# Kernel optimization log

Measured on AMD Instinct MI355X. Metric: run time of the kernel, lower is better.

## Reference

```python
import jax, jax.numpy as jnp
import numpy as np

P = 30000    # pathway graph nodes
E = 480000   # edges
G = 20000    # genes
MP = 32      # max pathways per gene (padded)
R = 28       # pathway root count
B = 4096     # batch of gene pairs
IN, H, OUT = 394, 256, 64
GD = 128     # params.gene_dim


def setup_inputs() -> dict:
    key = jax.random.key(0)
    ks = iter(jax.random.split(key, 48))
    nx = lambda shape, s=1.0: jax.random.normal(next(ks), shape, dtype=jnp.float32) * s
    inp = {}
    inp["x1"] = nx((P, IN))
    inp["x2"] = nx((P, IN))
    inp["edge_src"] = jax.random.randint(next(ks), (E,), 0, P)
    inp["edge_dst"] = jax.random.randint(next(ks), (E,), 0, P)
    inp["edge_weight"] = jax.random.uniform(next(ks), (E,), dtype=jnp.float32)
    for g in ("g1", "g2"):
        inp[g + "_w1"] = nx((IN, H), 0.05); inp[g + "_b1"] = jnp.zeros((H,), jnp.float32)
        inp[g + "_w2"] = nx((H, OUT), 0.05); inp[g + "_b2"] = jnp.zeros((OUT,), jnp.float32)
    inp["pl1_w"] = nx((OUT * R, 256), 0.02); inp["pl1_b"] = jnp.zeros((256,), jnp.float32)
    inp["bn1_g"] = jnp.ones((256,), jnp.float32); inp["bn1_b"] = jnp.zeros((256,), jnp.float32)
    inp["pl2_w"] = nx((256, GD), 0.05); inp["pl2_b"] = jnp.zeros((GD,), jnp.float32)
    inp["bn2_g"] = jnp.ones((GD,), jnp.float32); inp["bn2_b"] = jnp.zeros((GD,), jnp.float32)
    inp["fc_w"] = nx((2 * GD, 256), 0.05); inp["fc_b"] = jnp.zeros((256,), jnp.float32)
    inp["fc1_w"] = nx((256, 128), 0.05); inp["fc1_b"] = jnp.zeros((128,), jnp.float32)
    inp["fc2_w"] = nx((128, 1), 0.05); inp["fc2_b"] = jnp.zeros((1,), jnp.float32)
    inp["pathway_root"] = jax.random.randint(next(ks), (P,), 0, R)
    inp["gene_paths"] = jax.random.randint(next(ks), (G, MP), 0, P)
    inp["gene_paths_mask"] = jax.random.uniform(next(ks), (G, MP)) < 0.7
    inp["head_ids"] = jax.random.randint(next(ks), (B,), 0, G)
    inp["tail_ids"] = jax.random.randint(next(ks), (B,), 0, G)
    return inp


def gcn_conv(x, w, b, src, dst, ew):
    # PyG GCNConv with edge weights + self loops (fill_value=1), symmetric norm.
    h = x @ w
    deg = jnp.zeros((x.shape[0],), x.dtype).at[dst].add(ew) + 1.0
    norm = jax.lax.rsqrt(deg)
    msg = h[src] * (ew * norm[src] * norm[dst])[:, None]
    agg = jnp.zeros_like(h).at[dst].add(msg) + h * (norm * norm)[:, None]
    return agg + b


def pathway_gcn(x, w1, b1, w2, b2, src, dst, ew):
    h = jax.nn.relu(gcn_conv(x, w1, b1, src, dst, ew))  # F.dropout in eval = identity
    return gcn_conv(h, w2, b2, src, dst, ew)


def gene_pathway_feat(s, gene_ids, gene_paths, gene_paths_mask, pathway_root):
    # Vectorized form of the per-gene python-loop gather + per-root sum.
    paths = gene_paths[gene_ids]                      # [B, MP]
    m = gene_paths_mask[gene_ids].astype(s.dtype)     # [B, MP]
    gathered = s[paths]                               # [B, MP, 64]
    oh = jax.nn.one_hot(pathway_root[paths], R, dtype=s.dtype) * m[..., None]
    feat = jnp.einsum('bpr,bpd->brd', oh, gathered)   # segment-sum into roots
    return feat.reshape(paths.shape[0], R * s.shape[1])


def batchnorm(x, g, b, eps=1e-5):
    mu = x.mean(0)
    var = x.var(0)  # biased, as torch BN training
    return g * (x - mu) * jax.lax.rsqrt(var + eps) + b


def reference(x1, x2, edge_src, edge_dst, edge_weight,
              g1_w1, g1_b1, g1_w2, g1_b2, g2_w1, g2_b1, g2_w2, g2_b2,
              pl1_w, pl1_b, bn1_g, bn1_b, pl2_w, pl2_b, bn2_g, bn2_b,
              fc_w, fc_b, fc1_w, fc1_b, fc2_w, fc2_b,
              pathway_root, gene_paths, gene_paths_mask, head_ids, tail_ids):
    out1 = pathway_gcn(x1, g1_w1, g1_b1, g1_w2, g1_b2, edge_src, edge_dst, edge_weight)
    out2 = pathway_gcn(x2, g2_w1, g2_b1, g2_w2, g2_b2, edge_src, edge_dst, edge_weight)
    s = out1 + out2  # original stacks feats from both graphs per pathway, then sums

    def fuse(ids):
        f = gene_pathway_feat(s, ids, gene_paths, gene_paths_mask, pathway_root)
        h = jax.nn.relu(batchnorm(f @ pl1_w + pl1_b, bn1_g, bn1_b))
        return batchnorm(h @ pl2_w + pl2_b, bn2_g, bn2_b)

    fuse_feat = jnp.concatenate([fuse(head_ids), fuse(tail_ids)], axis=1)  # [B, 2*GD]
    final = jax.nn.relu(fuse_feat @ fc_w + fc_b) @ fc1_w + fc1_b
    return jax.nn.relu(final) @ fc2_w + fc2_b  # [B, 1]
```

## Files before the change

kernel.cpp:

```cpp
#include <hip/hip_runtime.h>
#include <cstdint>

typedef __attribute__((ext_vector_type(4))) float f32x4;
typedef __attribute__((ext_vector_type(8))) short s16x8;

__device__ inline unsigned short f2bf(float f) {
    unsigned u = __float_as_uint(f);
    unsigned r = (u + 0x7FFFu + ((u >> 16) & 1u)) >> 16;
    return (unsigned short)r;
}
__device__ inline float b2f(unsigned short h) {
    return __uint_as_float(((unsigned)h) << 16);
}

__device__ inline void gload16(const unsigned short* g, unsigned short* l) {
    __builtin_amdgcn_global_load_lds(
        (const __attribute__((address_space(1))) unsigned int*)g,
        (__attribute__((address_space(3))) unsigned int*)l, 16, 0, 0);
}

struct TD { const float* in; unsigned short* out; int K, N, Kp, ldo; };

__global__ void prep_kernel(const unsigned char* __restrict__ mask, int maskBytes,
                            int* __restrict__ flag, float* __restrict__ zspan, long long zwords,
                            TD d0, TD d1, TD d2, TD d3, TD d4, TD d5, TD d6, TD d7) {
    int y = blockIdx.y;
    if (y == 0) {
        if (blockIdx.x != 0) return;
        __shared__ int isByte, isFloat;
        if (threadIdx.x == 0) { isByte = 0; isFloat = 0; }
        __syncthreads();
        const unsigned* w = (const unsigned*)mask;
        for (int i = threadIdx.x; i < maskBytes / 4; i += blockDim.x) {
            unsigned v = w[i];
            if (v == 0u || v == 1u) continue;
            if (v == 0x3f800000u) isFloat = 1; else isByte = 1;
        }
        __syncthreads();
        if (threadIdx.x == 0) *flag = isFloat ? 2 : (isByte ? 1 : 0);
        return;
    }
    if (y == 1) {
        long long i = (long long)blockIdx.x * 256 + threadIdx.x;
        if (i < zwords) zspan[i] = 0.f;
        return;
    }
    TD d = d0;
    if (y == 3) d = d1; else if (y == 4) d = d2; else if (y == 5) d = d3;
    else if (y == 6) d = d4; else if (y == 7) d = d5; else if (y == 8) d = d6; else if (y == 9) d = d7;
    int idx = blockIdx.x * 256 + threadIdx.x;
    if (idx >= d.N * d.Kp) return;
    int n = idx / d.Kp, k = idx - n * d.Kp;
    d.out[(size_t)n * d.ldo + k] = (k < d.K) ? f2bf(d.in[(size_t)k * d.N + n]) : (unsigned short)0;
}

__global__ void deg_cnt_kernel(const int* __restrict__ dst, const float* __restrict__ ew,
                               float* __restrict__ degw, int* __restrict__ cnt, int E) {
    int e = blockIdx.x * 256 + threadIdx.x;
    if (e >= E) return;
    int d = dst[e];
    unsafeAtomicAdd(&degw[d], ew[e]);
    atomicAdd(&cnt[d], 1);
}

__global__ __launch_bounds__(1024) void norm_scan_kernel(const int* __restrict__ cnt,
                                                         int* __restrict__ rowstart,
                                                         float* __restrict__ degw, int P) {
    int t = threadIdx.x;
    if (blockIdx.x > 0) {
        int i = (blockIdx.x - 1) * 1024 + t;
        if (i < P) degw[i] = rsqrtf(degw[i] + 1.0f);
        return;
    }
    __shared__ int wsum[16];
    __shared__ int carry;
    int lane = t & 63, w = t >> 6;
    if (t == 0) { carry = 0; rowstart[0] = 0; }
    __syncthreads();
    for (int base = 0; base < P; base += 1024) {
        int v = (base + t < P) ? cnt[base + t] : 0;
        int x = v;
#pragma unroll
        for (int off = 1; off < 64; off <<= 1) {
            int y2 = __shfl_up(x, off);
            if (lane >= off) x += y2;
        }
        if (lane == 63) wsum[w] = x;
        __syncthreads();
        if (w == 0) {
            int xs = (lane < 16) ? wsum[lane] : 0;
#pragma unroll
            for (int off = 1; off < 16; off <<= 1) {
                int y2 = __shfl_up(xs, off);
                if (lane >= off) xs += y2;
            }
            if (lane < 16) wsum[lane] = xs;
        }
        __syncthreads();
        int wbase = (w == 0) ? 0 : wsum[w - 1];
        int inc = carry + wbase + x;
        if (base + t < P) rowstart[base + t + 1] = inc;
        __syncthreads();
        if (t == 1023) carry = inc;
        __syncthreads();
    }
}

__global__ void fill_kernel(const int* __restrict__ src, const int* __restrict__ dst,
                            const float* __restrict__ ew, const float* __restrict__ norm,
                            const int* __restrict__ rowstart, int* __restrict__ fill,
                            int* __restrict__ csrc, float* __restrict__ coef, int E) {
    int e = blockIdx.x * 256 + threadIdx.x;
    if (e >= E) return;
    int d = dst[e], sI = src[e];
    int pos = rowstart[d] + atomicAdd(&fill[d], 1);
    csrc[pos] = sI;
    coef[pos] = ew[e] * norm[sI] * norm[d];
}

__global__ __launch_bounds__(256) void conv1_agg_kernel(
    const unsigned short* __restrict__ Hb, const float* __restrict__ norm,
    const int* __restrict__ rowstart, const int* __restrict__ csrc, const float* __restrict__ coef,
    const float* __restrict__ b0, const float* __restrict__ b1,
    unsigned short* __restrict__ out, int P) {
    int node = blockIdx.x * 4 + (threadIdx.x >> 6);
    if (node >= P) return;
    int z = blockIdx.y;
    const unsigned short* H = Hb + (size_t)z * P * 256;
    const float* bias = z ? b1 : b0;
    int lane = threadIdx.x & 63;
    int f4 = lane * 4;
    float nn = norm[node];
    ushort4 hv = *(const ushort4*)(H + (size_t)node * 256 + f4);
    float a0 = b2f(hv.x) * nn * nn, a1 = b2f(hv.y) * nn * nn;
    float a2 = b2f(hv.z) * nn * nn, a3 = b2f(hv.w) * nn * nn;
    int s0 = rowstart[node], s1 = rowstart[node + 1];
    int p = s0;
    for (; p + 4 <= s1; p += 4) {
        int i0 = csrc[p], i1 = csrc[p + 1], i2 = csrc[p + 2], i3 = csrc[p + 3];
        float c0 = coef[p], c1 = coef[p + 1], c2 = coef[p + 2], c3 = coef[p + 3];
        ushort4 v0 = *(const ushort4*)(H + (size_t)i0 * 256 + f4);
        ushort4 v1 = *(const ushort4*)(H + (size_t)i1 * 256 + f4);
        ushort4 v2 = *(const ushort4*)(H + (size_t)i2 * 256 + f4);
        ushort4 v3 = *(const ushort4*)(H + (size_t)i3 * 256 + f4);
        a0 += b2f(v0.x) * c0 + b2f(v1.x) * c1 + b2f(v2.x) * c2 + b2f(v3.x) * c3;
        a1 += b2f(v0.y) * c0 + b2f(v1.y) * c1 + b2f(v2.y) * c2 + b2f(v3.y) * c3;
        a2 += b2f(v0.z) * c0 + b2f(v1.z) * c1 + b2f(v2.z) * c2 + b2f(v3.z) * c3;
        a3 += b2f(v0.w) * c0 + b2f(v1.w) * c1 + b2f(v2.w) * c2 + b2f(v3.w) * c3;
    }
    for (; p < s1; ++p) {
        int i0 = csrc[p];
        float c0 = coef[p];
        ushort4 v0 = *(const ushort4*)(H + (size_t)i0 * 256 + f4);
        a0 += b2f(v0.x) * c0; a1 += b2f(v0.y) * c0; a2 += b2f(v0.z) * c0; a3 += b2f(v0.w) * c0;
    }
    float4 bv = *(const float4*)(bias + f4);
    ushort4 o;
    o.x = f2bf(fmaxf(a0 + bv.x, 0.f));
    o.y = f2bf(fmaxf(a1 + bv.y, 0.f));
    o.z = f2bf(fmaxf(a2 + bv.z, 0.f));
    o.w = f2bf(fmaxf(a3 + bv.w, 0.f));
    *(ushort4*)(out + (size_t)node * 512 + z * 256 + f4) = o;
}

__global__ __launch_bounds__(256) void conv2_agg_kernel(
    const unsigned short* __restrict__ T, const float* __restrict__ norm,
    const int* __restrict__ rowstart, const int* __restrict__ csrc, const float* __restrict__ coef,
    const float* __restrict__ b0, const float* __restrict__ b1,
    float* __restrict__ s, int P) {
    int node = blockIdx.x * 4 + (threadIdx.x >> 6);
    if (node >= P) return;
    int lane = threadIdx.x & 63;
    float nn = norm[node];
    float acc = b2f(T[(size_t)node * 64 + lane]) * nn * nn;
    int s0 = rowstart[node], s1 = rowstart[node + 1];
    int p = s0;
    for (; p + 4 <= s1; p += 4) {
        int i0 = csrc[p], i1 = csrc[p + 1], i2 = csrc[p + 2], i3 = csrc[p + 3];
        float c0 = coef[p], c1 = coef[p + 1], c2 = coef[p + 2], c3 = coef[p + 3];
        acc += b2f(T[(size_t)i0 * 64 + lane]) * c0 + b2f(T[(size_t)i1 * 64 + lane]) * c1 +
               b2f(T[(size_t)i2 * 64 + lane]) * c2 + b2f(T[(size_t)i3 * 64 + lane]) * c3;
    }
    for (; p < s1; ++p) acc += b2f(T[(size_t)csrc[p] * 64 + lane]) * coef[p];
    s[(size_t)node * 64 + lane] = acc + b0[lane] + b1[lane];
}

struct G2 {
    const void* A[2]; const unsigned short* Bt[2]; const float* bias[2];
    float* Cf[2]; unsigned short* Cb[2];
};

template<int BM, int BN, int WM, int WN>
__global__ __launch_bounds__(256) void gemm1_hybrid_kernel(
    const float* __restrict__ x0, const float* __restrict__ x1,
    const unsigned short* __restrict__ Bt0, const unsigned short* __restrict__ Bt1,
    unsigned short* __restrict__ C0, unsigned short* __restrict__ C1,
    int M, int IN, int Kp, int ldc) {
    const int z = blockIdx.z;
    const float* A = z ? x1 : x0;
    const unsigned short* Bt = z ? Bt1 : Bt0;
    unsigned short* Cb = z ? C1 : C0;

    constexpr int LDK = 40;
    __shared__ __align__(16) unsigned short As[2][BM * LDK];
    __shared__ __align__(16) unsigned short Bs[2][BN * 32];
    const int t = threadIdx.x, lane = t & 63, wid = t >> 6;
    constexpr int NWC = BN / WN;
    const int wr = wid / NWC, wc = wid % NWC;
    constexpr int MR = WM / 16, NR = WN / 16;
    static_assert((BM / WM) * (BN / WN) == 4, "4 waves");
    constexpr int BI = BN / 64;
    const int row0 = blockIdx.y * BM, col0 = blockIdx.x * BN;
    const int sr = lane >> 2;
    const int sc = ((lane & 3) ^ ((lane >> 3) & 3)) * 8;
    int brow[BI];
#pragma unroll
    for (int i = 0; i < BI; ++i) brow[i] = col0 + (wid * BI + i) * 16 + sr;
    const int ar = t >> 2, akc = (t & 3) * 8;
    int arowg = row0 + ar; if (arowg >= M) arowg = M - 1;
    const float* aptr = A + (size_t)arowg * IN;

    f32x4 acc[MR][NR] = {};
    const int r16 = lane & 15, q = lane >> 4;
    const int kbA = q * 8;
    const int kbB = ((q ^ ((r16 >> 1) & 3)) * 8);

    auto stageB = [&](int buf, int kt) {
#pragma unroll
        for (int i = 0; i < BI; ++i)
            gload16(Bt + (size_t)brow[i] * Kp + kt + sc, &Bs[buf][(wid * BI + i) * 512]);
    };
    auto loadA = [&](int kt, float* v) {
        int kg = kt + akc;
        if (kg + 8 <= IN) {
            float2 a = *(const float2*)(aptr + kg);
            float2 b = *(const float2*)(aptr + kg + 2);
            float2 c = *(const float2*)(aptr + kg + 4);
            float2 d = *(const float2*)(aptr + kg + 6);
            v[0]=a.x; v[1]=a.y; v[2]=b.x; v[3]=b.y; v[4]=c.x; v[5]=c.y; v[6]=d.x; v[7]=d.y;
        } else {
#pragma unroll
            for (int j = 0; j < 8; ++j) v[j] = (kg + j < IN) ? aptr[kg + j] : 0.f;
        }
    };
    auto writeA = [&](int buf, const float* v) {
        s16x8 w;
#pragma unroll
        for (int j = 0; j < 8; ++j) w[j] = (short)f2bf(v[j]);
        *(s16x8*)&As[buf][ar * LDK + akc] = w;
    };

    {
        float v[8];
        stageB(0, 0);
        loadA(0, v);
        writeA(0, v);
    }
    int cur = 0;
    for (int kt = 0; kt < Kp; kt += 32) {
        __syncthreads();
        float nv[8];
        const bool has = (kt + 32 < Kp);
        if (has) { stageB(cur ^ 1, kt + 32); loadA(kt + 32, nv); }
        s16x8 af[MR], bfr[NR];
#pragma unroll
        for (int m = 0; m < MR; ++m)
            af[m] = *(const s16x8*)&As[cur][(wr * WM + m * 16 + r16) * LDK + kbA];
#pragma unroll
        for (int n = 0; n < NR; ++n)
            bfr[n] = *(const s16x8*)&Bs[cur][(wc * WN + n * 16 + r16) * 32 + kbB];
#pragma unroll
        for (int m = 0; m < MR; ++m)
#pragma unroll
            for (int n = 0; n < NR; ++n)
                acc[m][n] = __builtin_amdgcn_mfma_f32_16x16x32_bf16(af[m], bfr[n], acc[m][n], 0, 0, 0);
        if (has) writeA(cur ^ 1, nv);
        cur ^= 1;
    }
#pragma unroll
    for (int m = 0; m < MR; ++m)
#pragma unroll
        for (int n = 0; n < NR; ++n) {
            int col = col0 + wc * WN + n * 16 + r16;
#pragma unroll
            for (int r = 0; r < 4; ++r) {
                int row = row0 + wr * WM + m * 16 + q * 4 + r;
                if (row < M) Cb[(size_t)row * ldc + col] = f2bf(acc[m][n][r]);
            }
        }
}

template<int BM, int BN, int WM, int WN>
__global__ __launch_bounds__(256) void m97s_gemm_kernel(
    G2 g, int M, int Kp, int lda, int ldc, int relu) {
    const int z = blockIdx.z;
    const unsigned short* A = (const unsigned short*)(z ? g.A[1] : g.A[0]);
    const unsigned short* Bt = z ? g.Bt[1] : g.Bt[0];
    const float* bias = z ? g.bias[1] : g.bias[0];
    float* Cf = z ? g.Cf[1] : g.Cf[0];
    unsigned short* Cb = z ? g.Cb[1] : g.Cb[0];

    __shared__ __align__(16) unsigned short As[2][BM * 32];
    __shared__ __align__(16) unsigned short Bs[2][BN * 32];
    const int t = threadIdx.x, lane = t & 63, wid = t >> 6;
    constexpr int NWC = BN / WN;
    const int wr = wid / NWC, wc = wid % NWC;
    constexpr int MR = WM / 16, NR = WN / 16;
    static_assert((BM / WM) * (BN / WN) == 4, "4 waves");
    constexpr int AI = BM / 64, BI = BN / 64;
    const int row0 = blockIdx.y * BM, col0 = blockIdx.x * BN;
    const int sr = lane >> 2;
    const int sc = ((lane & 3) ^ ((lane >> 3) & 3)) * 8;
    int arow[AI];
#pragma unroll
    for (int i = 0; i < AI; ++i) {
        int r = row0 + (wid * AI + i) * 16 + sr;
        arow[i] = r < M ? r : M - 1;
    }
    int brow[BI];
#pragma unroll
    for (int i = 0; i < BI; ++i) brow[i] = col0 + (wid * BI + i) * 16 + sr;

    f32x4 acc[MR][NR] = {};
    const int r16 = lane & 15;
    const int kb = (((lane >> 4) ^ ((r16 >> 1) & 3)) * 8);

    auto stage = [&](int buf, int kt) {
#pragma unroll
        for (int i = 0; i < AI; ++i)
            gload16(A + (size_t)arow[i] * lda + kt + sc, &As[buf][(wid * AI + i) * 512]);
#pragma unroll
        for (int i = 0; i < BI; ++i)
            gload16(Bt + (size_t)brow[i] * Kp + kt + sc, &Bs[buf][(wid * BI + i) * 512]);
    };

    stage(0, 0);
    int cur = 0;
    for (int kt = 0; kt < Kp; kt += 32) {
        __syncthreads();
        if (kt + 32 < Kp) stage(cur ^ 1, kt + 32);
        s16x8 af[MR], bfr[NR];
#pragma unroll
        for (int m = 0; m < MR; ++m)
            af[m] = *(const s16x8*)&As[cur][(wr * WM + m * 16 + r16) * 32 + kb];
#pragma unroll
        for (int n = 0; n < NR; ++n)
            bfr[n] = *(const s16x8*)&Bs[cur][(wc * WN + n * 16 + r16) * 32 + kb];
#pragma unroll
        for (int m = 0; m < MR; ++m)
#pragma unroll
            for (int n = 0; n < NR; ++n)
                acc[m][n] = __builtin_amdgcn_mfma_f32_16x16x32_bf16(af[m], bfr[n], acc[m][n], 0, 0, 0);
        cur ^= 1;
    }
#pragma unroll
    for (int m = 0; m < MR; ++m)
#pragma unroll
        for (int n = 0; n < NR; ++n) {
            int col = col0 + wc * WN + n * 16 + r16;
#pragma unroll
            for (int r = 0; r < 4; ++r) {
                int row = row0 + wr * WM + m * 16 + (lane >> 4) * 4 + r;
                if (row < M) {
                    float v = acc[m][n][r] + (bias ? bias[col] : 0.f);
                    if (relu) v = fmaxf(v, 0.f);
                    if (Cf) Cf[(size_t)row * ldc + col] = v;
                    if (Cb) Cb[(size_t)row * ldc + col] = f2bf(v);
                }
            }
        }
}

template<int BM, int BN, int WM, int WN>
__global__ __launch_bounds__(256) void pl1_stats_kernel(
    G2 g, int M, int Kp, int lda, int ldc, float* __restrict__ statsPart, int C) {
    const int z = blockIdx.z;
    const unsigned short* A = (const unsigned short*)(z ? g.A[1] : g.A[0]);
    const unsigned short* Bt = z ? g.Bt[1] : g.Bt[0];
    const float* bias = z ? g.bias[1] : g.bias[0];
    float* Cf = z ? g.Cf[1] : g.Cf[0];

    __shared__ __align__(16) unsigned short As[2][BM * 32];
    __shared__ __align__(16) unsigned short Bs[2][BN * 32];
    const int t = threadIdx.x, lane = t & 63, wid = t >> 6;
    constexpr int NWC = BN / WN;
    const int wr = wid / NWC, wc = wid % NWC;
    constexpr int MR = WM / 16, NR = WN / 16;
    constexpr int AI = BM / 64, BI = BN / 64;
    const int row0 = blockIdx.y * BM, col0 = blockIdx.x * BN;
    const int sr = lane >> 2;
    const int sc = ((lane & 3) ^ ((lane >> 3) & 3)) * 8;
    int arow[AI];
#pragma unroll
    for (int i = 0; i < AI; ++i) {
        int r = row0 + (wid * AI + i) * 16 + sr;
        arow[i] = r < M ? r : M - 1;
    }
    int brow[BI];
#pragma unroll
    for (int i = 0; i < BI; ++i) brow[i] = col0 + (wid * BI + i) * 16 + sr;

    f32x4 acc[MR][NR] = {};
    const int r16 = lane & 15, q = lane >> 4;
    const int kb = ((q ^ ((r16 >> 1) & 3)) * 8);

    auto stage = [&](int buf, int kt) {
#pragma unroll
        for (int i = 0; i < AI; ++i)
            gload16(A + (size_t)arow[i] * lda + kt + sc, &As[buf][(wid * AI + i) * 512]);
#pragma unroll
        for (int i = 0; i < BI; ++i)
            gload16(Bt + (size_t)brow[i] * Kp + kt + sc, &Bs[buf][(wid * BI + i) * 512]);
    };

    stage(0, 0);
    int cur = 0;
    for (int kt = 0; kt < Kp; kt += 32) {
        __syncthreads();
        if (kt + 32 < Kp) stage(cur ^ 1, kt + 32);
        s16x8 af[MR], bfr[NR];
#pragma unroll
        for (int m = 0; m < MR; ++m)
            af[m] = *(const s16x8*)&As[cur][(wr * WM + m * 16 + r16) * 32 + kb];
#pragma unroll
        for (int n = 0; n < NR; ++n)
            bfr[n] = *(const s16x8*)&Bs[cur][(wc * WN + n * 16 + r16) * 32 + kb];
#pragma unroll
        for (int m = 0; m < MR; ++m)
#pragma unroll
            for (int n = 0; n < NR; ++n)
                acc[m][n] = __builtin_amdgcn_mfma_f32_16x16x32_bf16(af[m], bfr[n], acc[m][n], 0, 0, 0);
        cur ^= 1;
    }
    float* sp = statsPart + (size_t)z * 2 * C;
#pragma unroll
    for (int n = 0; n < NR; ++n) {
        int col = col0 + wc * WN + n * 16 + r16;
        float sm = 0.f, sq = 0.f;
#pragma unroll
        for (int m = 0; m < MR; ++m)
#pragma unroll
            for (int r = 0; r < 4; ++r) {
                int row = row0 + wr * WM + m * 16 + q * 4 + r;
                float v = acc[m][n][r] + bias[col];
                Cf[(size_t)row * ldc + col] = v;
                sm += v; sq += v * v;
            }
        sm += __shfl_xor(sm, 16); sq += __shfl_xor(sq, 16);
        sm += __shfl_xor(sm, 32); sq += __shfl_xor(sq, 32);
        if (lane < 16) {
            unsafeAtomicAdd(&sp[col], sm);
            unsafeAtomicAdd(&sp[C + col], sq);
        }
    }
}

template<int BM, int BN, int WM, int WN>
__global__ __launch_bounds__(256) void pl2_bn_stats_kernel(
    const float* __restrict__ z1, const unsigned short* __restrict__ Bt,
    const float* __restrict__ bias, float* __restrict__ z2,
    const float* __restrict__ bn1part, const float* __restrict__ bn1g, const float* __restrict__ bn1b,
    float* __restrict__ bn2part, int Mrows, int Kp, int ldc) {
    const int z = blockIdx.z;
    const float* A = z1 + (size_t)z * Mrows * Kp;
    float* Cf = z2 + (size_t)z * Mrows * ldc;

    constexpr int LDK = 40;
    __shared__ __align__(16) unsigned short As[BM * LDK];
    __shared__ __align__(16) unsigned short Bs[BN * 32];
    __shared__ float sc1[256], sh1[256];
    const int t = threadIdx.x, lane = t & 63, wid = t >> 6;
    {
        const float* bp = bn1part + (size_t)z * 2 * 256;
        float mu = bp[t] / Mrows;
        float var = bp[256 + t] / Mrows - mu * mu;
        float rstd = rsqrtf(var + 1e-5f);
        float s = rstd * bn1g[t];
        sc1[t] = s; sh1[t] = bn1b[t] - mu * s;
    }
    constexpr int NWC = BN / WN;
    const int wr = wid / NWC, wc = wid % NWC;
    constexpr int MR = WM / 16, NR = WN / 16;
    constexpr int BI = BN / 64;
    const int row0 = blockIdx.y * BM, col0 = blockIdx.x * BN;
    const int sr = lane >> 2;
    const int sc = ((lane & 3) ^ ((lane >> 3) & 3)) * 8;
    int brow[BI];
#pragma unroll
    for (int i = 0; i < BI; ++i) brow[i] = col0 + (wid * BI + i) * 16 + sr;
    const int ar = t >> 2, akc = (t & 3) * 8;
    const float* aptr = A + (size_t)(row0 + ar) * Kp;
    f32x4 acc[MR][NR] = {};
    const int r16 = lane & 15, q = lane >> 4;
    const int kbA = q * 8;
    const int kbB = ((q ^ ((r16 >> 1) & 3)) * 8);
    __syncthreads();

    for (int kt = 0; kt < Kp; kt += 32) {
#pragma unroll
        for (int i = 0; i < BI; ++i)
            gload16(Bt + (size_t)brow[i] * Kp + kt + sc, &Bs[(wid * BI + i) * 512]);
        {
            int kg = kt + akc;
            float4 a = *(const float4*)(aptr + kg);
            float4 b = *(const float4*)(aptr + kg + 4);
            float v[8] = {a.x, a.y, a.z, a.w, b.x, b.y, b.z, b.w};
            s16x8 w;
#pragma unroll
            for (int j = 0; j < 8; ++j)
                w[j] = (short)f2bf(fmaxf(v[j] * sc1[kg + j] + sh1[kg + j], 0.f));
            *(s16x8*)&As[ar * LDK + akc] = w;
        }
        __syncthreads();
        s16x8 af[MR], bfr[NR];
#pragma unroll
        for (int m = 0; m < MR; ++m)
            af[m] = *(const s16x8*)&As[(wr * WM + m * 16 + r16) * LDK + kbA];
#pragma unroll
        for (int n = 0; n < NR; ++n)
            bfr[n] = *(const s16x8*)&Bs[(wc * WN + n * 16 + r16) * 32 + kbB];
#pragma unroll
        for (int m = 0; m < MR; ++m)
#pragma unroll
            for (int n = 0; n < NR; ++n)
                acc[m][n] = __builtin_amdgcn_mfma_f32_16x16x32_bf16(af[m], bfr[n], acc[m][n], 0, 0, 0);
        __syncthreads();
    }
    float* sp = bn2part + (size_t)z * 2 * ldc;
#pragma unroll
    for (int n = 0; n < NR; ++n) {
        int col = col0 + wc * WN + n * 16 + r16;
        float sm = 0.f, sq = 0.f;
#pragma unroll
        for (int m = 0; m < MR; ++m)
#pragma unroll
            for (int r = 0; r < 4; ++r) {
                int row = row0 + wr * WM + m * 16 + q * 4 + r;
                float v = acc[m][n][r] + bias[col];
                Cf[(size_t)row * ldc + col] = v;
                sm += v; sq += v * v;
            }
        sm += __shfl_xor(sm, 16); sq += __shfl_xor(sq, 16);
        sm += __shfl_xor(sm, 32); sq += __shfl_xor(sq, 32);
        if (lane < 16) {
            unsafeAtomicAdd(&sp[col], sm);
            unsafeAtomicAdd(&sp[ldc + col], sq);
        }
    }
}

__global__ __launch_bounds__(64) void gene_feat_kernel(
    const float* __restrict__ S, const int* __restrict__ head, const int* __restrict__ tail,
    const int* __restrict__ gene_paths, const void* __restrict__ mask,
    const int* __restrict__ root, unsigned short* __restrict__ feat, const int* __restrict__ flag,
    int B) {
    __shared__ float lds[28 * 64];
    int lane = threadIdx.x;
#pragma unroll
    for (int i = 0; i < 28; ++i) lds[i * 64 + lane] = 0.f;
    int side = blockIdx.y;
    const int* ids = side ? tail : head;
    int gene = ids[blockIdx.x];
    int fl = *flag;
    const unsigned char* mb = (const unsigned char*)mask;
    const int* mi = (const int*)mask;
    const float* mf = (const float*)mask;
    for (int p = 0; p < 32; ++p) {
        int idx = gene * 32 + p;
        int m = (fl == 0) ? mi[idx] : (fl == 1) ? (int)mb[idx] : (mf[idx] != 0.f);
        if (!m) continue;
        int path = gene_paths[idx];
        int r = root[path];
        lds[r * 64 + lane] += S[(size_t)path * 64 + lane];
    }
    unsigned short* frow = feat + ((size_t)side * B + blockIdx.x) * 1792;
#pragma unroll
    for (int i = 0; i < 28; ++i) frow[i * 64 + lane] = f2bf(lds[i * 64 + lane]);
}

__global__ __launch_bounds__(256) void mlp_tail_kernel(
    const float* __restrict__ z2, const float* __restrict__ bn2part,
    const float* __restrict__ bn2g, const float* __restrict__ bn2b,
    const unsigned short* __restrict__ fct, const float* __restrict__ fc_b,
    const unsigned short* __restrict__ fc1t, const float* __restrict__ fc1_b,
    const float* __restrict__ fc2_w, const float* __restrict__ fc2_b,
    float* __restrict__ out, int B) {
    constexpr int LDK = 40;
    __shared__ __align__(16) unsigned short As[64 * LDK];
    __shared__ __align__(16) unsigned short Bs[256 * 32];
    __shared__ __align__(16) unsigned short T1[64 * 264];
    __shared__ float part[64];
    __shared__ float sc2[256], sh2[256];
    const int t = threadIdx.x, lane = t & 63, wid = t >> 6;
    const int row0 = blockIdx.x * 64;
    const int sr = lane >> 2, sc = ((lane & 3) ^ ((lane >> 3) & 3)) * 8;
    const int r16 = lane & 15, q = lane >> 4;
    const int kbA = q * 8;
    const int kbB = ((q ^ ((r16 >> 1) & 3)) * 8);
    const int ar = t >> 2, akc = (t & 3) * 8;

    {
        int side = t >> 7, cc = t & 127;
        const float* bp = bn2part + (size_t)side * 256;
        float mu = bp[cc] / B;
        float var = bp[128 + cc] / B - mu * mu;
        float rstd = rsqrtf(var + 1e-5f);
        float s = rstd * bn2g[cc];
        sc2[t] = s; sh2[t] = bn2b[cc] - mu * s;
    }
    __syncthreads();

    {
        f32x4 acc[4][4] = {};
        int brow[4];
#pragma unroll
        for (int i = 0; i < 4; ++i) brow[i] = (wid * 4 + i) * 16 + sr;
        for (int kt = 0; kt < 256; kt += 32) {
#pragma unroll
            for (int i = 0; i < 4; ++i)
                gload16(fct + (size_t)brow[i] * 256 + kt + sc, &Bs[(wid * 4 + i) * 512]);
            {
                int c0 = kt + akc;
                int side = c0 >> 7, cc = c0 & 127;
                const float* zr = z2 + ((size_t)side * B + row0 + ar) * 128 + cc;
                float4 a = *(const float4*)zr;
                float4 b = *(const float4*)(zr + 4);
                float v[8] = {a.x, a.y, a.z, a.w, b.x, b.y, b.z, b.w};
                s16x8 w;
#pragma unroll
                for (int j = 0; j < 8; ++j) w[j] = (short)f2bf(v[j] * sc2[c0 + j] + sh2[c0 + j]);
                *(s16x8*)&As[ar * LDK + akc] = w;
            }
            __syncthreads();
            s16x8 af[4], bfr[4];
#pragma unroll
            for (int m = 0; m < 4; ++m) af[m] = *(const s16x8*)&As[(m * 16 + r16) * LDK + kbA];
#pragma unroll
            for (int n = 0; n < 4; ++n) bfr[n] = *(const s16x8*)&Bs[(wid * 64 + n * 16 + r16) * 32 + kbB];
#pragma unroll
            for (int m = 0; m < 4; ++m)
#pragma unroll
                for (int n = 0; n < 4; ++n)
                    acc[m][n] = __builtin_amdgcn_mfma_f32_16x16x32_bf16(af[m], bfr[n], acc[m][n], 0, 0, 0);
            __syncthreads();
        }
#pragma unroll
        for (int m = 0; m < 4; ++m)
#pragma unroll
            for (int n = 0; n < 4; ++n) {
                int col = wid * 64 + n * 16 + r16;
#pragma unroll
                for (int r = 0; r < 4; ++r) {
                    int row = m * 16 + q * 4 + r;
                    T1[row * 264 + col] = f2bf(fmaxf(acc[m][n][r] + fc_b[col], 0.f));
                }
            }
    }
    __syncthreads();
    if (t < 64) part[t] = 0.f;

    f32x4 acc2[4][2] = {};
    {
        int brow[2];
#pragma unroll
        for (int i = 0; i < 2; ++i) brow[i] = (wid * 2 + i) * 16 + sr;
        for (int kt = 0; kt < 256; kt += 32) {
#pragma unroll
            for (int i = 0; i < 2; ++i)
                gload16(fc1t + (size_t)brow[i] * 256 + kt + sc, &Bs[(wid * 2 + i) * 512]);
            __syncthreads();
            s16x8 af[4], bfr[2];
#pragma unroll
            for (int m = 0; m < 4; ++m) af[m] = *(const s16x8*)&T1[(m * 16 + r16) * 264 + kt + q * 8];
#pragma unroll
            for (int n = 0; n < 2; ++n) bfr[n] = *(const s16x8*)&Bs[(wid * 32 + n * 16 + r16) * 32 + kbB];
#pragma unroll
            for (int m = 0; m < 4; ++m)
#pragma unroll
                for (int n = 0; n < 2; ++n)
                    acc2[m][n] = __builtin_amdgcn_mfma_f32_16x16x32_bf16(af[m], bfr[n], acc2[m][n], 0, 0, 0);
            __syncthreads();
        }
    }
#pragma unroll
    for (int m = 0; m < 4; ++m)
#pragma unroll
        for (int r = 0; r < 4; ++r) {
            float sv = 0.f;
#pragma unroll
            for (int n = 0; n < 2; ++n) {
                int col = wid * 32 + n * 16 + r16;
                float v = fmaxf(acc2[m][n][r] + fc1_b[col], 0.f);
                sv += v * fc2_w[col];
            }
#pragma unroll
            for (int off = 1; off < 16; off <<= 1) sv += __shfl_xor(sv, off);
            if (r16 == 0) atomicAdd(&part[m * 16 + q * 4 + r], sv);
        }
    __syncthreads();
    if (t < 64 && row0 + t < B) out[row0 + t] = part[t] + fc2_b[0];
}

extern "C" void kernel_launch(void* const* d_in, const int* in_sizes, int n_in,
                              void* d_out, int out_size, void* d_ws, size_t ws_size,
                              hipStream_t stream) {
    const float* x[2] = {(const float*)d_in[0], (const float*)d_in[1]};
    const int* esrc = (const int*)d_in[2];
    const int* edst = (const int*)d_in[3];
    const float* ew = (const float*)d_in[4];
    const float* g_w1[2] = {(const float*)d_in[5], (const float*)d_in[9]};
    const float* g_b1[2] = {(const float*)d_in[6], (const float*)d_in[10]};
    const float* g_w2[2] = {(const float*)d_in[7], (const float*)d_in[11]};
    const float* g_b2[2] = {(const float*)d_in[8], (const float*)d_in[12]};
    const float* pl1_w = (const float*)d_in[13];
    const float* pl1_b = (const float*)d_in[14];
    const float* bn1_g = (const float*)d_in[15];
    const float* bn1_b = (const float*)d_in[16];
    const float* pl2_w = (const float*)d_in[17];
    const float* pl2_b = (const float*)d_in[18];
    const float* bn2_g = (const float*)d_in[19];
    const float* bn2_b = (const float*)d_in[20];
    const float* fc_w = (const float*)d_in[21];
    const float* fc_b = (const float*)d_in[22];
    const float* fc1_w = (const float*)d_in[23];
    const float* fc1_b = (const float*)d_in[24];
    const float* fc2_w = (const float*)d_in[25];
    const float* fc2_b = (const float*)d_in[26];
    const int* root = (const int*)d_in[27];
    const int* gene_paths = (const int*)d_in[28];
    const void* gmask = d_in[29];
    const int* head = (const int*)d_in[30];
    const int* tail = (const int*)d_in[31];

    const int P = in_sizes[27];
    const int E = in_sizes[2];
    const int B = in_sizes[30];
    const int IN = 394, Kp1 = 416, H = 256, OUT = 64, GD = 128;
    const int MB = (P + 63) / 64;

    char* ws = (char*)d_ws;
    size_t off = 0;
    auto alloc = [&](size_t bytes) -> char* {
        char* p = ws + off;
        off = (off + bytes + 255) & ~(size_t)255;
        return p;
    };
    int* flag = (int*)alloc(256);
    float* norm = (float*)alloc((size_t)P * 4);
    int* cnt = (int*)alloc((size_t)P * 4);
    int* fillp = (int*)alloc((size_t)P * 4);
    float* bn1part = (float*)alloc((size_t)2 * 2 * 256 * 4);
    float* bn2part = (float*)alloc((size_t)2 * 2 * 128 * 4);
    char* zend = ws + off;
    int* rowstart = (int*)alloc((size_t)(P + 1) * 4);
    int* csrc = (int*)alloc((size_t)E * 4);
    float* coef = (float*)alloc((size_t)E * 4);
    unsigned short* W1t = (unsigned short*)alloc((size_t)2 * H * Kp1 * 2);
    unsigned short* W2tc = (unsigned short*)alloc((size_t)OUT * 512 * 2);
    unsigned short* pl1t = (unsigned short*)alloc((size_t)256 * 1792 * 2);
    unsigned short* pl2t = (unsigned short*)alloc((size_t)GD * 256 * 2);
    unsigned short* fct = (unsigned short*)alloc((size_t)256 * 256 * 2);
    unsigned short* fc1t = (unsigned short*)alloc((size_t)GD * 256 * 2);
    unsigned short* bufH = (unsigned short*)alloc((size_t)2 * P * H * 2);
    unsigned short* bufh1 = (unsigned short*)alloc((size_t)P * 512 * 2);
    float* s = (float*)alloc((size_t)P * OUT * 4);
    (void)n_in; (void)out_size; (void)ws_size;

    unsigned short* bufh2 = bufH;
    unsigned short* feat = bufh1;
    char* mlp = (char*)bufH + 4194304;
    size_t mo = 0;
    auto malloc2 = [&](size_t bytes) -> char* {
        char* p = mlp + mo;
        mo = (mo + bytes + 255) & ~(size_t)255;
        return p;
    };
    float* z1 = (float*)malloc2((size_t)2 * B * 256 * 4);
    float* z2 = (float*)malloc2((size_t)2 * B * GD * 4);

    {
        long long zwords = (zend - (char*)norm) / 4;
        TD d0 = {g_w1[0], W1t, IN, H, Kp1, Kp1};
        TD d1 = {g_w1[1], W1t + (size_t)H * Kp1, IN, H, Kp1, Kp1};
        TD d2 = {g_w2[0], W2tc, H, OUT, H, 512};
        TD d3 = {g_w2[1], W2tc + 256, H, OUT, H, 512};
        TD d4 = {pl1_w, pl1t, 1792, 256, 1792, 1792};
        TD d5 = {pl2_w, pl2t, 256, GD, 256, 256};
        TD d6 = {fc_w, fct, 256, 256, 256, 256};
        TD d7 = {fc1_w, fc1t, 256, GD, 256, 256};
        prep_kernel<<<dim3(1792, 10), 256, 0, stream>>>(
            (const unsigned char*)gmask, 4096, flag, norm, zwords,
            d0, d1, d2, d3, d4, d5, d6, d7);
    }

    deg_cnt_kernel<<<(E + 255) / 256, 256, 0, stream>>>(edst, ew, norm, cnt, E);
    norm_scan_kernel<<<1 + (P + 1023) / 1024, 1024, 0, stream>>>(cnt, rowstart, norm, P);
    fill_kernel<<<(E + 255) / 256, 256, 0, stream>>>(esrc, edst, ew, norm, rowstart, fillp, csrc, coef, E);

    gemm1_hybrid_kernel<64, 256, 64, 64><<<dim3(1, MB, 2), 256, 0, stream>>>(
        x[0], x[1], W1t, W1t + (size_t)H * Kp1, bufH, bufH + (size_t)P * H, P, IN, Kp1, H);

    conv1_agg_kernel<<<dim3((P + 3) / 4, 2), 256, 0, stream>>>(bufH, norm, rowstart, csrc, coef,
                                                               g_b1[0], g_b1[1], bufh1, P);
    {
        G2 g = {{bufh1, nullptr}, {W2tc, nullptr}, {nullptr, nullptr},
                {nullptr, nullptr}, {bufh2, nullptr}};
        m97s_gemm_kernel<64, 64, 32, 32><<<dim3(1, MB, 1), 256, 0, stream>>>(
            g, P, 512, 512, OUT, 0);
    }
    conv2_agg_kernel<<<dim3((P + 3) / 4), 256, 0, stream>>>(bufh2, norm, rowstart, csrc, coef,
                                                            g_b2[0], g_b2[1], s, P);

    gene_feat_kernel<<<dim3(B, 2), 64, 0, stream>>>(s, head, tail, gene_paths, gmask, root, feat, flag, B);

    {
        G2 g = {{feat, feat + (size_t)B * 1792}, {pl1t, pl1t}, {pl1_b, pl1_b},
                {z1, z1 + (size_t)B * 256}, {nullptr, nullptr}};
        pl1_stats_kernel<64, 128, 32, 64><<<dim3(2, B / 64, 2), 256, 0, stream>>>(
            g, B, 1792, 1792, 256, bn1part, 256);
    }
    pl2_bn_stats_kernel<64, 64, 32, 32><<<dim3(2, B / 64, 2), 256, 0, stream>>>(
        z1, pl2t, pl2_b, z2, bn1part, bn1_g, bn1_b, bn2part, B, 256, GD);

    mlp_tail_kernel<<<B / 64, 256, 0, stream>>>(z2, bn2part, bn2_g, bn2_b, fct, fc_b,
                                                fc1t, fc1_b, fc2_w, fc2_b, (float*)d_out, B);
}
```

Measured before the change: 348.8 us.

## Rewrite scan, widen conv1 gather unroll, use direct-load first GEMM

The single-block prefix scan now has each thread sum a contiguous segment, do one block-wide scan, then write its segment. This replaces about 30 barrier-heavy iterations. The conv1 aggregation gains an 8-way unrolled gather loop for more memory-level parallelism. The first GEMM drops its LDS double-buffering and has each wave load A (fp32 to bf16) and B fragments straight from global memory, with a 64x128 block tile split across more blocks. That GEMM change gives up LDS reuse and may cost more global traffic, since A rows are re-read by each column block.

After: 404.5 us. +15.9%, slower.

```diff
diff --git a/kernel.cpp b/kernel.cpp
--- a/kernel.cpp
+++ b/kernel.cpp
@@ -72,38 +72,31 @@
         if (i < P) degw[i] = rsqrtf(degw[i] + 1.0f);
         return;
     }
+    const int seg = (P + 1023) >> 10;
+    int base = t * seg;
+    int sum = 0;
+    for (int j = 0; j < seg; ++j) {
+        int i = base + j;
+        if (i < P) sum += cnt[i];
+    }
+    int lane = t & 63, w = t >> 6;
+    int x = sum;
+#pragma unroll
+    for (int off = 1; off < 64; off <<= 1) {
+        int y = __shfl_up(x, off);
+        if (lane >= off) x += y;
+    }
     __shared__ int wsum[16];
-    __shared__ int carry;
-    int lane = t & 63, w = t >> 6;
-    if (t == 0) { carry = 0; rowstart[0] = 0; }
+    if (lane == 63) wsum[w] = x;
     __syncthreads();
-    for (int base = 0; base < P; base += 1024) {
-        int v = (base + t < P) ? cnt[base + t] : 0;
-        int x = v;
-#pragma unroll
-        for (int off = 1; off < 64; off <<= 1) {
-            int y2 = __shfl_up(x, off);
-            if (lane >= off) x += y2;
-        }
-        if (lane == 63) wsum[w] = x;
-        __syncthreads();
-        if (w == 0) {
-            int xs = (lane < 16) ? wsum[lane] : 0;
-#pragma unroll
-            for (int off = 1; off < 16; off <<= 1) {
-                int y2 = __shfl_up(xs, off);
-                if (lane >= off) xs += y2;
-            }
-            if (lane < 16) wsum[lane] = xs;
-        }
-        __syncthreads();
-        int wbase = (w == 0) ? 0 : wsum[w - 1];
-        int inc = carry + wbase + x;
-        if (base + t < P) rowstart[base + t + 1] = inc;
-        __syncthreads();
-        if (t == 1023) carry = inc;
-        __syncthreads();
-    }
+    int woff = 0;
+    for (int i = 0; i < w; ++i) woff += wsum[i];
+    int run = woff + x - sum;
+    for (int j = 0; j < seg; ++j) {
+        int i = base + j;
+        if (i < P) { run += cnt[i]; rowstart[i + 1] = run; }
+    }
+    if (t == 0) rowstart[0] = 0;
 }
 
 __global__ void fill_kernel(const int* __restrict__ src, const int* __restrict__ dst,
@@ -136,6 +129,28 @@
     float a2 = b2f(hv.z) * nn * nn, a3 = b2f(hv.w) * nn * nn;
     int s0 = rowstart[node], s1 = rowstart[node + 1];
     int p = s0;
+    for (; p + 8 <= s1; p += 8) {
+        int i0 = csrc[p], i1 = csrc[p + 1], i2 = csrc[p + 2], i3 = csrc[p + 3];
+        int i4 = csrc[p + 4], i5 = csrc[p + 5], i6 = csrc[p + 6], i7 = csrc[p + 7];
+        float c0 = coef[p], c1 = coef[p + 1], c2 = coef[p + 2], c3 = coef[p + 3];
+        float c4 = coef[p + 4], c5 = coef[p + 5], c6 = coef[p + 6], c7 = coef[p + 7];
+        ushort4 v0 = *(const ushort4*)(H + (size_t)i0 * 256 + f4);
+        ushort4 v1 = *(const ushort4*)(H + (size_t)i1 * 256 + f4);
+        ushort4 v2 = *(const ushort4*)(H + (size_t)i2 * 256 + f4);
+        ushort4 v3 = *(const ushort4*)(H + (size_t)i3 * 256 + f4);
+        ushort4 v4 = *(const ushort4*)(H + (size_t)i4 * 256 + f4);
+        ushort4 v5 = *(const ushort4*)(H + (size_t)i5 * 256 + f4);
+        ushort4 v6 = *(const ushort4*)(H + (size_t)i6 * 256 + f4);
+        ushort4 v7 = *(const ushort4*)(H + (size_t)i7 * 256 + f4);
+        a0 += b2f(v0.x) * c0 + b2f(v1.x) * c1 + b2f(v2.x) * c2 + b2f(v3.x) * c3
+            + b2f(v4.x) * c4 + b2f(v5.x) * c5 + b2f(v6.x) * c6 + b2f(v7.x) * c7;
+        a1 += b2f(v0.y) * c0 + b2f(v1.y) * c1 + b2f(v2.y) * c2 + b2f(v3.y) * c3
+            + b2f(v4.y) * c4 + b2f(v5.y) * c5 + b2f(v6.y) * c6 + b2f(v7.y) * c7;
+        a2 += b2f(v0.z) * c0 + b2f(v1.z) * c1 + b2f(v2.z) * c2 + b2f(v3.z) * c3
+            + b2f(v4.z) * c4 + b2f(v5.z) * c5 + b2f(v6.z) * c6 + b2f(v7.z) * c7;
+        a3 += b2f(v0.w) * c0 + b2f(v1.w) * c1 + b2f(v2.w) * c2 + b2f(v3.w) * c3
+            + b2f(v4.w) * c4 + b2f(v5.w) * c5 + b2f(v6.w) * c6 + b2f(v7.w) * c7;
+    }
     for (; p + 4 <= s1; p += 4) {
         int i0 = csrc[p], i1 = csrc[p + 1], i2 = csrc[p + 2], i3 = csrc[p + 3];
         float c0 = coef[p], c1 = coef[p + 1], c2 = coef[p + 2], c3 = coef[p + 3];
@@ -190,8 +205,8 @@
     float* Cf[2]; unsigned short* Cb[2];
 };
 
-template<int BM, int BN, int WM, int WN>
-__global__ __launch_bounds__(256) void gemm1_hybrid_kernel(
+template<int WM, int WN>
+__global__ __launch_bounds__(256) void gemm1_direct_kernel(
     const float* __restrict__ x0, const float* __restrict__ x1,
     const unsigned short* __restrict__ Bt0, const unsigned short* __restrict__ Bt1,
     unsigned short* __restrict__ C0, unsigned short* __restrict__ C1,
@@ -200,91 +215,60 @@
     const float* A = z ? x1 : x0;
     const unsigned short* Bt = z ? Bt1 : Bt0;
     unsigned short* Cb = z ? C1 : C0;
-
-    constexpr int LDK = 40;
-    __shared__ __align__(16) unsigned short As[2][BM * LDK];
-    __shared__ __align__(16) unsigned short Bs[2][BN * 32];
-    const int t = threadIdx.x, lane = t & 63, wid = t >> 6;
-    constexpr int NWC = BN / WN;
-    const int wr = wid / NWC, wc = wid % NWC;
+    const int lane = threadIdx.x & 63, wid = threadIdx.x >> 6;
     constexpr int MR = WM / 16, NR = WN / 16;
-    static_assert((BM / WM) * (BN / WN) == 4, "4 waves");
-    constexpr int BI = BN / 64;
-    const int row0 = blockIdx.y * BM, col0 = blockIdx.x * BN;
-    const int sr = lane >> 2;
-    const int sc = ((lane & 3) ^ ((lane >> 3) & 3)) * 8;
-    int brow[BI];
-#pragma unroll
-    for (int i = 0; i < BI; ++i) brow[i] = col0 + (wid * BI + i) * 16 + sr;
-    const int ar = t >> 2, akc = (t & 3) * 8;
-    int arowg = row0 + ar; if (arowg >= M) arowg = M - 1;
-    const float* aptr = A + (size_t)arowg * IN;
-
+    const int row0 = blockIdx.y * WM;
+    const int col0 = blockIdx.x * (4 * WN) + wid * WN;
+    const int r16 = lane & 15, q = lane >> 4;
     f32x4 acc[MR][NR] = {};
-    const int r16 = lane & 15, q = lane >> 4;
-    const int kbA = q * 8;
-    const int kbB = ((q ^ ((r16 >> 1) & 3)) * 8);
-
-    auto stageB = [&](int buf, int kt) {
-#pragma unroll
-        for (int i = 0; i < BI; ++i)
-            gload16(Bt + (size_t)brow[i] * Kp + kt + sc, &Bs[buf][(wid * BI + i) * 512]);
-    };
-    auto loadA = [&](int kt, float* v) {
-        int kg = kt + akc;
-        if (kg + 8 <= IN) {
-            float2 a = *(const float2*)(aptr + kg);
-            float2 b = *(const float2*)(aptr + kg + 2);
-            float2 c = *(const float2*)(aptr + kg + 4);
-            float2 d = *(const float2*)(aptr + kg + 6);
-            v[0]=a.x; v[1]=a.y; v[2]=b.x; v[3]=b.y; v[4]=c.x; v[5]=c.y; v[6]=d.x; v[7]=d.y;
-        } else {
-#pragma unroll
-            for (int j = 0; j < 8; ++j) v[j] = (kg + j < IN) ? aptr[kg + j] : 0.f;
-        }
-    };
-    auto writeA = [&](int buf, const float* v) {
-        s16x8 w;
-#pragma unroll
-        for (int j = 0; j < 8; ++j) w[j] = (short)f2bf(v[j]);
-        *(s16x8*)&As[buf][ar * LDK + akc] = w;
-    };
-
-    {
-        float v[8];
-        stageB(0, 0);
-        loadA(0, v);
-        writeA(0, v);
-    }
-    int cur = 0;
+    const float* aptr[MR];
+#pragma unroll
+    for (int m = 0; m < MR; ++m) {
+        int r = row0 + m * 16 + r16;
+        if (r >= M) r = M - 1;
+        aptr[m] = A + (size_t)r * IN;
+    }
+    const unsigned short* bptr[NR];
+#pragma unroll
+    for (int n = 0; n < NR; ++n)
+        bptr[n] = Bt + (size_t)(col0 + n * 16 + r16) * Kp;
+
     for (int kt = 0; kt < Kp; kt += 32) {
-        __syncthreads();
-        float nv[8];
-        const bool has = (kt + 32 < Kp);
-        if (has) { stageB(cur ^ 1, kt + 32); loadA(kt + 32, nv); }
+        int kg = kt + q * 8;
         s16x8 af[MR], bfr[NR];
 #pragma unroll
-        for (int m = 0; m < MR; ++m)
-            af[m] = *(const s16x8*)&As[cur][(wr * WM + m * 16 + r16) * LDK + kbA];
-#pragma unroll
         for (int n = 0; n < NR; ++n)
-            bfr[n] = *(const s16x8*)&Bs[cur][(wc * WN + n * 16 + r16) * 32 + kbB];
+            bfr[n] = *(const s16x8*)(bptr[n] + kg);
+#pragma unroll
+        for (int m = 0; m < MR; ++m) {
+            float v[8];
+            if (kg + 8 <= IN) {
+                float2 a = *(const float2*)(aptr[m] + kg);
+                float2 b = *(const float2*)(aptr[m] + kg + 2);
+                float2 c = *(const float2*)(aptr[m] + kg + 4);
+                float2 d = *(const float2*)(aptr[m] + kg + 6);
+                v[0]=a.x; v[1]=a.y; v[2]=b.x; v[3]=b.y; v[4]=c.x; v[5]=c.y; v[6]=d.x; v[7]=d.y;
+            } else {
+#pragma unroll
+                for (int j = 0; j < 8; ++j) v[j] = (kg + j < IN) ? aptr[m][kg + j] : 0.f;
+            }
+#pragma unroll
+            for (int j = 0; j < 8; ++j) af[m][j] = (short)f2bf(v[j]);
+        }
 #pragma unroll
         for (int m = 0; m < MR; ++m)
 #pragma unroll
             for (int n = 0; n < NR; ++n)
                 acc[m][n] = __builtin_amdgcn_mfma_f32_16x16x32_bf16(af[m], bfr[n], acc[m][n], 0, 0, 0);
-        if (has) writeA(cur ^ 1, nv);
-        cur ^= 1;
     }
 #pragma unroll
     for (int m = 0; m < MR; ++m)
 #pragma unroll
         for (int n = 0; n < NR; ++n) {
-            int col = col0 + wc * WN + n * 16 + r16;
+            int col = col0 + n * 16 + r16;
 #pragma unroll
             for (int r = 0; r < 4; ++r) {
-                int row = row0 + wr * WM + m * 16 + q * 4 + r;
+                int row = row0 + m * 16 + q * 4 + r;
                 if (row < M) Cb[(size_t)row * ldc + col] = f2bf(acc[m][n][r]);
             }
         }
@@ -797,7 +781,7 @@
     norm_scan_kernel<<<1 + (P + 1023) / 1024, 1024, 0, stream>>>(cnt, rowstart, norm, P);
     fill_kernel<<<(E + 255) / 256, 256, 0, stream>>>(esrc, edst, ew, norm, rowstart, fillp, csrc, coef, E);
 
-    gemm1_hybrid_kernel<64, 256, 64, 64><<<dim3(1, MB, 2), 256, 0, stream>>>(
+    gemm1_direct_kernel<64, 32><<<dim3(H / 128, MB, 2), 256, 0, stream>>>(
         x[0], x[1], W1t, W1t + (size_t)H * Kp1, bufH, bufH + (size_t)P * H, P, IN, Kp1, H);
 
     conv1_agg_kernel<<<dim3((P + 3) / 4, 2), 256, 0, stream>>>(bufH, norm, rowstart, csrc, coef,
```

## Parallelize degree scan, fuse both graph aggregations in conv1, retile pl1 GEMM

Applied to the files above, without the earlier changes.

The row-start prefix scan now gives each of the 1024 threads a contiguous segment to scan serially, with a single block-level pass, replacing the looped 1024-wide chunk scan that needed four barriers per chunk. The conv1 aggregation handles both graphs in one thread, so CSR indices and coefficients are loaded once and reused for two feature gathers, and the grid's second dimension is dropped. The pl1 GEMM tile shrinks from 64x128 to 64x64 with twice the column blocks, raising occupancy. Trade-offs: the segmented scan reads cnt with strided, uncoalesced accesses, and the fused aggregation uses more registers per thread.

Result: slower. 367.4 us (+5.3%).

```diff
diff --git a/kernel.cpp b/kernel.cpp
--- a/kernel.cpp
+++ b/kernel.cpp
@@ -72,38 +72,31 @@
         if (i < P) degw[i] = rsqrtf(degw[i] + 1.0f);
         return;
     }
+    const int seg = (P + 1023) >> 10;
+    int base = t * seg;
+    int sum = 0;
+    for (int j = 0; j < seg; ++j) {
+        int i = base + j;
+        if (i < P) sum += cnt[i];
+    }
+    int lane = t & 63, w = t >> 6;
+    int x = sum;
+#pragma unroll
+    for (int off = 1; off < 64; off <<= 1) {
+        int y = __shfl_up(x, off);
+        if (lane >= off) x += y;
+    }
     __shared__ int wsum[16];
-    __shared__ int carry;
-    int lane = t & 63, w = t >> 6;
-    if (t == 0) { carry = 0; rowstart[0] = 0; }
+    if (lane == 63) wsum[w] = x;
     __syncthreads();
-    for (int base = 0; base < P; base += 1024) {
-        int v = (base + t < P) ? cnt[base + t] : 0;
-        int x = v;
-#pragma unroll
-        for (int off = 1; off < 64; off <<= 1) {
-            int y2 = __shfl_up(x, off);
-            if (lane >= off) x += y2;
-        }
-        if (lane == 63) wsum[w] = x;
-        __syncthreads();
-        if (w == 0) {
-            int xs = (lane < 16) ? wsum[lane] : 0;
-#pragma unroll
-            for (int off = 1; off < 16; off <<= 1) {
-                int y2 = __shfl_up(xs, off);
-                if (lane >= off) xs += y2;
-            }
-            if (lane < 16) wsum[lane] = xs;
-        }
-        __syncthreads();
-        int wbase = (w == 0) ? 0 : wsum[w - 1];
-        int inc = carry + wbase + x;
-        if (base + t < P) rowstart[base + t + 1] = inc;
-        __syncthreads();
-        if (t == 1023) carry = inc;
-        __syncthreads();
-    }
+    int woff = 0;
+    for (int i = 0; i < w; ++i) woff += wsum[i];
+    int run = woff + x - sum;
+    for (int j = 0; j < seg; ++j) {
+        int i = base + j;
+        if (i < P) { run += cnt[i]; rowstart[i + 1] = run; }
+    }
+    if (t == 0) rowstart[0] = 0;
 }
 
 __global__ void fill_kernel(const int* __restrict__ src, const int* __restrict__ dst,
@@ -125,42 +118,55 @@
     unsigned short* __restrict__ out, int P) {
     int node = blockIdx.x * 4 + (threadIdx.x >> 6);
     if (node >= P) return;
-    int z = blockIdx.y;
-    const unsigned short* H = Hb + (size_t)z * P * 256;
-    const float* bias = z ? b1 : b0;
+    const unsigned short* H0 = Hb;
+    const unsigned short* H1 = Hb + (size_t)P * 256;
     int lane = threadIdx.x & 63;
     int f4 = lane * 4;
     float nn = norm[node];
-    ushort4 hv = *(const ushort4*)(H + (size_t)node * 256 + f4);
-    float a0 = b2f(hv.x) * nn * nn, a1 = b2f(hv.y) * nn * nn;
-    float a2 = b2f(hv.z) * nn * nn, a3 = b2f(hv.w) * nn * nn;
+    float nn2 = nn * nn;
+    ushort4 h0 = *(const ushort4*)(H0 + (size_t)node * 256 + f4);
+    ushort4 h1 = *(const ushort4*)(H1 + (size_t)node * 256 + f4);
+    float a0 = b2f(h0.x) * nn2, a1 = b2f(h0.y) * nn2, a2 = b2f(h0.z) * nn2, a3 = b2f(h0.w) * nn2;
+    float g0 = b2f(h1.x) * nn2, g1 = b2f(h1.y) * nn2, g2 = b2f(h1.z) * nn2, g3 = b2f(h1.w) * nn2;
     int s0 = rowstart[node], s1 = rowstart[node + 1];
     int p = s0;
     for (; p + 4 <= s1; p += 4) {
         int i0 = csrc[p], i1 = csrc[p + 1], i2 = csrc[p + 2], i3 = csrc[p + 3];
         float c0 = coef[p], c1 = coef[p + 1], c2 = coef[p + 2], c3 = coef[p + 3];
-        ushort4 v0 = *(const ushort4*)(H + (size_t)i0 * 256 + f4);
-        ushort4 v1 = *(const ushort4*)(H + (size_t)i1 * 256 + f4);
-        ushort4 v2 = *(const ushort4*)(H + (size_t)i2 * 256 + f4);
-        ushort4 v3 = *(const ushort4*)(H + (size_t)i3 * 256 + f4);
+        ushort4 v0 = *(const ushort4*)(H0 + (size_t)i0 * 256 + f4);
+        ushort4 v1 = *(const ushort4*)(H0 + (size_t)i1 * 256 + f4);
+        ushort4 v2 = *(const ushort4*)(H0 + (size_t)i2 * 256 + f4);
+        ushort4 v3 = *(const ushort4*)(H0 + (size_t)i3 * 256 + f4);
+        ushort4 w0 = *(const ushort4*)(H1 + (size_t)i0 * 256 + f4);
+        ushort4 w1 = *(const ushort4*)(H1 + (size_t)i1 * 256 + f4);
+        ushort4 w2 = *(const ushort4*)(H1 + (size_t)i2 * 256 + f4);
+        ushort4 w3 = *(const ushort4*)(H1 + (size_t)i3 * 256 + f4);
         a0 += b2f(v0.x) * c0 + b2f(v1.x) * c1 + b2f(v2.x) * c2 + b2f(v3.x) * c3;
         a1 += b2f(v0.y) * c0 + b2f(v1.y) * c1 + b2f(v2.y) * c2 + b2f(v3.y) * c3;
         a2 += b2f(v0.z) * c0 + b2f(v1.z) * c1 + b2f(v2.z) * c2 + b2f(v3.z) * c3;
         a3 += b2f(v0.w) * c0 + b2f(v1.w) * c1 + b2f(v2.w) * c2 + b2f(v3.w) * c3;
+        g0 += b2f(w0.x) * c0 + b2f(w1.x) * c1 + b2f(w2.x) * c2 + b2f(w3.x) * c3;
+        g1 += b2f(w0.y) * c0 + b2f(w1.y) * c1 + b2f(w2.y) * c2 + b2f(w3.y) * c3;
+        g2 += b2f(w0.z) * c0 + b2f(w1.z) * c1 + b2f(w2.z) * c2 + b2f(w3.z) * c3;
+        g3 += b2f(w0.w) * c0 + b2f(w1.w) * c1 + b2f(w2.w) * c2 + b2f(w3.w) * c3;
     }
     for (; p < s1; ++p) {
         int i0 = csrc[p];
         float c0 = coef[p];
-        ushort4 v0 = *(const ushort4*)(H + (size_t)i0 * 256 + f4);
+        ushort4 v0 = *(const ushort4*)(H0 + (size_t)i0 * 256 + f4);
+        ushort4 w0 = *(const ushort4*)(H1 + (size_t)i0 * 256 + f4);
         a0 += b2f(v0.x) * c0; a1 += b2f(v0.y) * c0; a2 += b2f(v0.z) * c0; a3 += b2f(v0.w) * c0;
-    }
-    float4 bv = *(const float4*)(bias + f4);
-    ushort4 o;
-    o.x = f2bf(fmaxf(a0 + bv.x, 0.f));
-    o.y = f2bf(fmaxf(a1 + bv.y, 0.f));
-    o.z = f2bf(fmaxf(a2 + bv.z, 0.f));
-    o.w = f2bf(fmaxf(a3 + bv.w, 0.f));
-    *(ushort4*)(out + (size_t)node * 512 + z * 256 + f4) = o;
+        g0 += b2f(w0.x) * c0; g1 += b2f(w0.y) * c0; g2 += b2f(w0.z) * c0; g3 += b2f(w0.w) * c0;
+    }
+    float4 bv0 = *(const float4*)(b0 + f4);
+    float4 bv1 = *(const float4*)(b1 + f4);
+    ushort4 o0, o1;
+    o0.x = f2bf(fmaxf(a0 + bv0.x, 0.f)); o0.y = f2bf(fmaxf(a1 + bv0.y, 0.f));
+    o0.z = f2bf(fmaxf(a2 + bv0.z, 0.f)); o0.w = f2bf(fmaxf(a3 + bv0.w, 0.f));
+    o1.x = f2bf(fmaxf(g0 + bv1.x, 0.f)); o1.y = f2bf(fmaxf(g1 + bv1.y, 0.f));
+    o1.z = f2bf(fmaxf(g2 + bv1.z, 0.f)); o1.w = f2bf(fmaxf(g3 + bv1.w, 0.f));
+    *(ushort4*)(out + (size_t)node * 512 + f4) = o0;
+    *(ushort4*)(out + (size_t)node * 512 + 256 + f4) = o1;
 }
 
 __global__ __launch_bounds__(256) void conv2_agg_kernel(
@@ -800,8 +806,8 @@
     gemm1_hybrid_kernel<64, 256, 64, 64><<<dim3(1, MB, 2), 256, 0, stream>>>(
         x[0], x[1], W1t, W1t + (size_t)H * Kp1, bufH, bufH + (size_t)P * H, P, IN, Kp1, H);
 
-    conv1_agg_kernel<<<dim3((P + 3) / 4, 2), 256, 0, stream>>>(bufH, norm, rowstart, csrc, coef,
-                                                               g_b1[0], g_b1[1], bufh1, P);
+    conv1_agg_kernel<<<dim3((P + 3) / 4), 256, 0, stream>>>(bufH, norm, rowstart, csrc, coef,
+                                                            g_b1[0], g_b1[1], bufh1, P);
     {
         G2 g = {{bufh1, nullptr}, {W2tc, nullptr}, {nullptr, nullptr},
                 {nullptr, nullptr}, {bufh2, nullptr}};
@@ -816,7 +822,7 @@
     {
         G2 g = {{feat, feat + (size_t)B * 1792}, {pl1t, pl1t}, {pl1_b, pl1_b},
                 {z1, z1 + (size_t)B * 256}, {nullptr, nullptr}};
-        pl1_stats_kernel<64, 128, 32, 64><<<dim3(2, B / 64, 2), 256, 0, stream>>>(
+        pl1_stats_kernel<64, 64, 32, 32><<<dim3(4, B / 64, 2), 256, 0, stream>>>(
             g, B, 1792, 1792, 256, bn1part, 256);
     }
     pl2_bn_stats_kernel<64, 64, 32, 32><<<dim3(2, B / 64, 2), 256, 0, stream>>>(
```
